# Kernel tuning notes

Hardware: AMD Instinct MI355X
Metric: run time of the kernel (lower is better)

## Reference

```python
import jax, jax.numpy as jnp
import numpy as np

# module hyperparams (init_kwargs)
OUTLINER_RATIO_1 = 0.01
OUTLINER_RATIO_2 = 0.01
SUB_OUTLINER_RATIO_2 = 0.2
SUB_OUTLINER_BIT_2 = 8
RANK = 16


def setup_inputs() -> dict:
    key = jax.random.key(0)
    k1, k2 = jax.random.split(key)
    B, H, S, D = 2, 16, 2048, 128
    # x1 is a softmax output (attention probabilities): rows sum to 1, values in [0,1]
    logits = jax.random.normal(k1, (B, H, S, S), dtype=jnp.float32)
    x1 = jax.nn.softmax(logits, axis=-1)
    x2 = jax.random.normal(k2, (B, H, S, D), dtype=jnp.float32)
    return {"x1": x1, "x2": x2}


def get_statistics_softmax(x, outliner_ratio):
    # kth-value threshold on first batch element (torch.kthvalue, 1-indexed)
    v = jnp.sort(x[0].reshape(-1))
    k = int(v.size * (1.0 - outliner_ratio))
    return v[k - 1]


def get_statistics_x2(x, outliner_ratio, sub_ratio, bit):
    x0 = x[0]  # [H, S, D]
    D = x0.shape[-1]
    a = jnp.abs(x0).reshape(-1)
    k = int(a.size * (1.0 - outliner_ratio))
    outliner = jnp.sort(a)[k - 1]
    # residual after removing outliers; rank columns by L2 norm
    resid = jnp.where(jnp.abs(x0) > outliner, 0.0, x0).reshape(-1, D)
    col_norm = jnp.linalg.norm(resid, axis=0)  # [D]
    n_cols = max(1, int(sub_ratio * D))
    _, cols = jax.lax.top_k(col_norm, n_cols)  # max-norm column list (static size)
    sub = resid[:, cols]
    qmax = float(2 ** (bit - 1) - 1)
    scale = jnp.max(jnp.abs(sub)) / qmax
    return outliner, cols, scale


def prune_softmax(x, outliner):
    return jnp.where(x > outliner, x, 0.0)


def fake_divide_outliner_suboutlinear_svd(x, outliner, cols, scale, rank, bit):
    # 1) split out outliers (kept exactly)
    x_out = jnp.where(jnp.abs(x) > outliner, x, 0.0)
    r = x - x_out
    # 2) rank-`rank` SVD approximation of the residual (batched over B,H)
    U, Sv, Vt = jnp.linalg.svd(r, full_matrices=False)
    x_lr = (U[..., :rank] * Sv[..., None, :rank]) @ Vt[..., :rank, :]
    r2 = r - x_lr
    # 3) fake-quantize the high-norm (sub-outlier) columns at `bit` bits; drop the rest
    qmax = float(2 ** (bit - 1) - 1)
    sub_q = jnp.clip(jnp.round(r2[..., cols] / scale), -qmax - 1.0, qmax) * scale
    r_q = jnp.zeros_like(r2).at[..., cols].set(sub_q)
    return x_out + x_lr + r_q


def reference(x1, x2):
    # iteration = 0 (< 10): compute statistics branch of EfficientMemoryGEMMWithSoftmaxFunc.forward
    result = x1 @ x2
    outliner_1 = get_statistics_softmax(x1, OUTLINER_RATIO_1)
    outliner_2, cols_2, scale_2 = get_statistics_x2(
        x2, OUTLINER_RATIO_2, SUB_OUTLINER_RATIO_2, SUB_OUTLINER_BIT_2)
    # The pruned/compressed tensors are computed (saved for backward in torch);
    # forward output matches Func.forward's returns.
    _x1p = prune_softmax(x1, outliner_1)
    _x2c = fake_divide_outliner_suboutlinear_svd(
        x2, outliner_2, cols_2, scale_2, RANK, SUB_OUTLINER_BIT_2)
    return (result, outliner_1, outliner_2, cols_2, scale_2)
```

## Files before the change

kernel.cpp:

```cpp
#include <hip/hip_runtime.h>

typedef __bf16 bf16x8 __attribute__((ext_vector_type(8)));
typedef unsigned short u16x8 __attribute__((ext_vector_type(8)));
typedef float f32x4 __attribute__((ext_vector_type(4)));

#define S_DIM 2048
#define D_DIM 128
#define N1 67108864LL
#define N2 4194304LL
#define RANK1 66437774u
#define RANK2 4152359u

#define OUT_O1 8388608
#define OUT_O2 8388609
#define OUT_COLS 8388610
#define OUT_SCALE 8388635

#define WS_H0 0
#define WS_H1 2048
#define WS_H2 4096
#define WS_H3 6144
#define WS_STATE 6656
#define WS_SMAX 6660
#define WS_MASK 6664
#define WS_SUMSQ 6672
#define WS_TOTAL 8192

__device__ __forceinline__ unsigned short f2bf(float f) {
  unsigned u = __float_as_uint(f);
  return (unsigned short)((u + 0x7FFFu + ((u >> 16) & 1u)) >> 16);
}

__global__ void init_ws(unsigned* __restrict__ ws) {
  int i = blockIdx.x * 256 + threadIdx.x;
  if (i < WS_TOTAL) ws[i] = (i == WS_STATE) ? RANK2 : 0u;
}

#define LDA 40

__global__ __launch_bounds__(256, 2) void gemm_kernel(
    const float* __restrict__ x1, const float* __restrict__ x2,
    float* __restrict__ out) {
  __shared__ __align__(16) unsigned short lA[128 * LDA];
  __shared__ __align__(16) unsigned short lB[128 * LDA];

  const int bh = blockIdx.x >> 4;
  const int mt = blockIdx.x & 15;
  const int t = threadIdx.x;
  const int lane = t & 63;
  const int wave = t >> 6;
  const int wm = (wave >> 1) * 64;
  const int wn = (wave & 1) * 64;
  const int l15 = lane & 15;
  const int quad = lane >> 4;

  const float* Ag = x1 + (long long)bh * S_DIM * S_DIM + (long long)mt * 128 * S_DIM;
  const float* Bg = x2 + (long long)bh * S_DIM * D_DIM;
  float* Cg = out + (long long)bh * S_DIM * D_DIM + (long long)mt * 128 * D_DIM;

  f32x4 acc[4][4];
#pragma unroll
  for (int i = 0; i < 4; ++i)
#pragma unroll
    for (int j = 0; j < 4; ++j) acc[i][j] = f32x4{0.f, 0.f, 0.f, 0.f};

  const int a_seg = t & 7;
  const int a_row = t >> 3;
  const int b_n = t & 127;
  const int b_kq = t >> 7;

  for (int kb = 0; kb < S_DIM; kb += 32) {
    __syncthreads();
#pragma unroll
    for (int p = 0; p < 4; ++p) {
      int row = a_row + p * 32;
      float4 v = *reinterpret_cast<const float4*>(Ag + (long long)row * S_DIM + kb + a_seg * 4);
      unsigned long long pk = (unsigned long long)f2bf(v.x)
                            | ((unsigned long long)f2bf(v.y) << 16)
                            | ((unsigned long long)f2bf(v.z) << 32)
                            | ((unsigned long long)f2bf(v.w) << 48);
      *reinterpret_cast<unsigned long long*>(&lA[row * LDA + a_seg * 4]) = pk;
    }
#pragma unroll
    for (int g = 0; g < 4; ++g) {
      int k0 = b_kq * 16 + g * 4;
      long long base = (long long)(kb + k0) * D_DIM + b_n;
      float f0 = Bg[base];
      float f1 = Bg[base + D_DIM];
      float f2 = Bg[base + 2 * D_DIM];
      float f3 = Bg[base + 3 * D_DIM];
      unsigned long long pk = (unsigned long long)f2bf(f0)
                            | ((unsigned long long)f2bf(f1) << 16)
                            | ((unsigned long long)f2bf(f2) << 32)
                            | ((unsigned long long)f2bf(f3) << 48);
      *reinterpret_cast<unsigned long long*>(&lB[b_n * LDA + k0]) = pk;
    }
    __syncthreads();

    bf16x8 af[4], bfr[4];
#pragma unroll
    for (int i = 0; i < 4; ++i) {
      af[i] = __builtin_bit_cast(bf16x8,
          *reinterpret_cast<const u16x8*>(&lA[(wm + i * 16 + l15) * LDA + quad * 8]));
      bfr[i] = __builtin_bit_cast(bf16x8,
          *reinterpret_cast<const u16x8*>(&lB[(wn + i * 16 + l15) * LDA + quad * 8]));
    }
#pragma unroll
    for (int i = 0; i < 4; ++i)
#pragma unroll
      for (int j = 0; j < 4; ++j)
        acc[i][j] = __builtin_amdgcn_mfma_f32_16x16x32_bf16(af[i], bfr[j], acc[i][j], 0, 0, 0);
  }

#pragma unroll
  for (int i = 0; i < 4; ++i) {
#pragma unroll
    for (int j = 0; j < 4; ++j) {
      int row0 = wm + i * 16 + quad * 4;
      int col = wn + j * 16 + l15;
#pragma unroll
      for (int r = 0; r < 4; ++r)
        Cg[(long long)(row0 + r) * D_DIM + col] = acc[i][j][r];
    }
  }
}

__global__ void x1_hist(const float* __restrict__ x1, unsigned* __restrict__ hist) {
  __shared__ unsigned lh[4 * 2049];
  for (int i = threadIdx.x; i < 4 * 2049; i += 256) lh[i] = 0u;
  __syncthreads();
  const int sub = (threadIdx.x & 3) * 2049;
  long long i0 = (long long)(blockIdx.x * 256 + threadIdx.x) * 4;
  long long stride = (long long)gridDim.x * 1024;
  for (long long i = i0; i < N1; i += stride) {
    float4 v = *reinterpret_cast<const float4*>(x1 + i);
    atomicAdd(&lh[sub + (__float_as_uint(v.x) >> 19)], 1u);
    atomicAdd(&lh[sub + (__float_as_uint(v.y) >> 19)], 1u);
    atomicAdd(&lh[sub + (__float_as_uint(v.z) >> 19)], 1u);
    atomicAdd(&lh[sub + (__float_as_uint(v.w) >> 19)], 1u);
  }
  __syncthreads();
  for (int i = threadIdx.x; i < 2048; i += 256) {
    unsigned s = lh[i] + lh[2049 + i] + lh[2 * 2049 + i] + lh[3 * 2049 + i];
    if (s) atomicAdd(&hist[i], s);
  }
}

__global__ void x1_select(const unsigned* __restrict__ hist, float* __restrict__ out) {
  __shared__ unsigned ps[256];
  const int t = threadIdx.x;
  unsigned v[8];
  unsigned s = 0;
#pragma unroll
  for (int j = 0; j < 8; ++j) { v[j] = hist[t * 8 + j]; s += v[j]; }
  ps[t] = s;
  __syncthreads();
  for (int off = 1; off < 256; off <<= 1) {
    unsigned add = (t >= off) ? ps[t - off] : 0u;
    __syncthreads();
    ps[t] += add;
    __syncthreads();
  }
  unsigned incl = ps[t];
  unsigned before = incl - s;
  if (RANK1 >= before && RANK1 < incl) {
    unsigned rr = RANK1 - before;
    for (int j = 0; j < 8; ++j) {
      if (rr < v[j]) {
        unsigned b = (unsigned)(t * 8 + j);
        float lo = __uint_as_float(b << 19);
        float hi = __uint_as_float((b + 1u) << 19);
        out[OUT_O1] = lo + (hi - lo) * (((float)rr + 0.5f) / (float)v[j]);
        break;
      }
      rr -= v[j];
    }
  }
}

__global__ void x2_hist(const float* __restrict__ x2, unsigned* __restrict__ h,
                        const unsigned* __restrict__ state, int phase) {
  __shared__ unsigned lh[2048];
  const int nb = (phase == 3) ? 512 : 2048;
  for (int i = threadIdx.x; i < nb; i += 256) lh[i] = 0u;
  __syncthreads();
  const unsigned b1 = state[1];
  const unsigned pfx2 = (state[1] << 11) | state[2];
  long long i0 = (long long)(blockIdx.x * 256 + threadIdx.x) * 4;
  long long stride = (long long)gridDim.x * 1024;
  for (long long i = i0; i < N2; i += stride) {
    float4 v = *reinterpret_cast<const float4*>(x2 + i);
    float fv[4] = {v.x, v.y, v.z, v.w};
#pragma unroll
    for (int j = 0; j < 4; ++j) {
      unsigned key = __float_as_uint(fv[j]) & 0x7FFFFFFFu;
      if (phase == 1) {
        atomicAdd(&lh[key >> 20], 1u);
      } else if (phase == 2) {
        if ((key >> 20) == b1) atomicAdd(&lh[(key >> 9) & 0x7FFu], 1u);
      } else {
        if ((key >> 9) == pfx2) atomicAdd(&lh[key & 0x1FFu], 1u);
      }
    }
  }
  __syncthreads();
  for (int i = threadIdx.x; i < nb; i += 256)
    if (lh[i]) atomicAdd(&h[i], lh[i]);
}

__global__ void x2_scan(const unsigned* __restrict__ h, unsigned* state,
                        float* __restrict__ out, int phase) {
  __shared__ unsigned ps[256];
  const int nb = (phase == 3) ? 512 : 2048;
  const int per = nb >> 8;
  const int t = threadIdx.x;
  const unsigned r = state[0];
  const unsigned sb1 = state[1];
  const unsigned sb2 = state[2];
  unsigned v[8];
  unsigned s = 0;
  for (int j = 0; j < per; ++j) { v[j] = h[t * per + j]; s += v[j]; }
  ps[t] = s;
  __syncthreads();
  for (int off = 1; off < 256; off <<= 1) {
    unsigned add = (t >= off) ? ps[t - off] : 0u;
    __syncthreads();
    ps[t] += add;
    __syncthreads();
  }
  unsigned incl = ps[t];
  unsigned before = incl - s;
  if (r >= before && r < incl) {
    unsigned rr = r - before;
    for (int j = 0; j < per; ++j) {
      if (rr < v[j]) {
        unsigned b = (unsigned)(t * per + j);
        state[0] = rr;
        if (phase == 1) state[1] = b;
        else if (phase == 2) state[2] = b;
        else {
          unsigned bits = (sb1 << 20) | (sb2 << 9) | b;
          state[3] = bits;
          out[OUT_O2] = __uint_as_float(bits);
        }
        break;
      }
      rr -= v[j];
    }
  }
}

__global__ void colnorm_kernel(const float* __restrict__ x2,
                               const unsigned* __restrict__ state,
                               float* __restrict__ sumsq) {
  const float thr = __uint_as_float(state[3]);
  const int t = threadIdx.x;
  const int c = t & 127;
  const int half = t >> 7;
  float local = 0.f;
  for (int i = 0; i < 64; ++i) {
    int row = blockIdx.x * 128 + i * 2 + half;
    float x = x2[(long long)row * 128 + c];
    if (fabsf(x) <= thr) local += x * x;
  }
  __shared__ float red[256];
  red[t] = local;
  __syncthreads();
  if (half == 0) atomicAdd(&sumsq[c], red[c] + red[c + 128]);
}

__global__ void topk_kernel(const float* __restrict__ sumsq, float* __restrict__ out,
                            unsigned* __restrict__ mask) {
  __shared__ float v[128];
  __shared__ float rv[128];
  __shared__ int ri[128];
  __shared__ unsigned msk[4];
  const int t = threadIdx.x;
  v[t] = sumsq[t];
  if (t < 4) msk[t] = 0u;
  __syncthreads();
  for (int s = 0; s < 25; ++s) {
    rv[t] = v[t];
    ri[t] = t;
    __syncthreads();
    for (int off = 64; off >= 1; off >>= 1) {
      if (t < off) {
        float a = rv[t], b = rv[t + off];
        int ia = ri[t], ib = ri[t + off];
        if (b > a || (b == a && ib < ia)) { rv[t] = b; ri[t] = ib; }
      }
      __syncthreads();
    }
    if (t == 0) {
      int c = ri[0];
      out[OUT_COLS + s] = (float)c;
      v[c] = -1.0f;
      msk[c >> 5] |= 1u << (c & 31);
    }
    __syncthreads();
  }
  if (t < 4) mask[t] = msk[t];
}

__global__ void scale_kernel(const float* __restrict__ x2,
                             const unsigned* __restrict__ state,
                             const unsigned* __restrict__ mask,
                             unsigned* __restrict__ smax) {
  const float thr = __uint_as_float(state[3]);
  unsigned long long mlo = (unsigned long long)mask[0] | ((unsigned long long)mask[1] << 32);
  unsigned long long mhi = (unsigned long long)mask[2] | ((unsigned long long)mask[3] << 32);
  long long i0 = (long long)(blockIdx.x * 256 + threadIdx.x) * 4;
  long long stride = (long long)gridDim.x * 1024;
  float best = 0.f;
  for (long long i = i0; i < N2; i += stride) {
    float4 v = *reinterpret_cast<const float4*>(x2 + i);
    float fv[4] = {v.x, v.y, v.z, v.w};
    int cbase = (int)(i & 127);
#pragma unroll
    for (int j = 0; j < 4; ++j) {
      int c = cbase + j;
      unsigned long long w = (c < 64) ? mlo : mhi;
      if ((w >> (c & 63)) & 1ULL) {
        float a = fabsf(fv[j]);
        if (a <= thr && a > best) best = a;
      }
    }
  }
  __shared__ float red[256];
  red[threadIdx.x] = best;
  __syncthreads();
  for (int off = 128; off >= 1; off >>= 1) {
    if (threadIdx.x < off) red[threadIdx.x] = fmaxf(red[threadIdx.x], red[threadIdx.x + off]);
    __syncthreads();
  }
  if (threadIdx.x == 0) atomicMax(smax, __float_as_uint(red[0]));
}

__global__ void finalize_kernel(const unsigned* __restrict__ smax, float* __restrict__ out) {
  out[OUT_SCALE] = __uint_as_float(*smax) / 127.0f;
}

extern "C" void kernel_launch(void* const* d_in, const int* in_sizes, int n_in,
                              void* d_out, int out_size, void* d_ws, size_t ws_size,
                              hipStream_t stream) {
  (void)in_sizes; (void)n_in; (void)out_size; (void)ws_size;
  const float* x1 = (const float*)d_in[0];
  const float* x2 = (const float*)d_in[1];
  float* out = (float*)d_out;
  unsigned* ws = (unsigned*)d_ws;

  init_ws<<<32, 256, 0, stream>>>(ws);
  gemm_kernel<<<512, 256, 0, stream>>>(x1, x2, out);
  x1_hist<<<512, 256, 0, stream>>>(x1, ws + WS_H0);
  x1_select<<<1, 256, 0, stream>>>(ws + WS_H0, out);
  x2_hist<<<256, 256, 0, stream>>>(x2, ws + WS_H1, ws + WS_STATE, 1);
  x2_scan<<<1, 256, 0, stream>>>(ws + WS_H1, ws + WS_STATE, out, 1);
  x2_hist<<<256, 256, 0, stream>>>(x2, ws + WS_H2, ws + WS_STATE, 2);
  x2_scan<<<1, 256, 0, stream>>>(ws + WS_H2, ws + WS_STATE, out, 2);
  x2_hist<<<256, 256, 0, stream>>>(x2, ws + WS_H3, ws + WS_STATE, 3);
  x2_scan<<<1, 256, 0, stream>>>(ws + WS_H3, ws + WS_STATE, out, 3);
  colnorm_kernel<<<256, 256, 0, stream>>>(x2, ws + WS_STATE, (float*)(ws + WS_SUMSQ));
  topk_kernel<<<1, 128, 0, stream>>>((const float*)(ws + WS_SUMSQ), out, ws + WS_MASK);
  scale_kernel<<<256, 256, 0, stream>>>(x2, ws + WS_STATE, ws + WS_MASK, ws + WS_SMAX);
  finalize_kernel<<<1, 1, 0, stream>>>(ws + WS_SMAX, out);
}
```

Measured before the change: 928.6 us.

## Fuse x1 histogram into GEMM, prefetch next tiles into registers, swizzle block order

Builds the x1 value histogram inside the GEMM kernel for the first batch element, from the A-tile registers already loaded. This removes the separate pass that re-read the whole 256MB x1 tensor. The GEMM now register-prefetches the next k-slice of A and B while computing the current one, and remaps block indices so that blocks sharing a tile are grouped. The cost is 32KB of extra shared memory for per-wave histograms, which may reduce occupancy, and LDS atomics added to the GEMM inner loop.

After: 843.4 us. -9.2%, faster.

```diff
diff --git a/kernel.cpp b/kernel.cpp
--- a/kernel.cpp
+++ b/kernel.cpp
@@ -31,6 +31,13 @@
   return (unsigned short)((u + 0x7FFFu + ((u >> 16) & 1u)) >> 16);
 }
 
+__device__ __forceinline__ unsigned long long pack4(float x, float y, float z, float w) {
+  return (unsigned long long)f2bf(x)
+       | ((unsigned long long)f2bf(y) << 16)
+       | ((unsigned long long)f2bf(z) << 32)
+       | ((unsigned long long)f2bf(w) << 48);
+}
+
 __global__ void init_ws(unsigned* __restrict__ ws) {
   int i = blockIdx.x * 256 + threadIdx.x;
   if (i < WS_TOTAL) ws[i] = (i == WS_STATE) ? RANK2 : 0u;
@@ -40,12 +47,14 @@
 
 __global__ __launch_bounds__(256, 2) void gemm_kernel(
     const float* __restrict__ x1, const float* __restrict__ x2,
-    float* __restrict__ out) {
+    float* __restrict__ out, unsigned* __restrict__ hist) {
   __shared__ __align__(16) unsigned short lA[128 * LDA];
   __shared__ __align__(16) unsigned short lB[128 * LDA];
-
-  const int bh = blockIdx.x >> 4;
-  const int mt = blockIdx.x & 15;
+  __shared__ unsigned lh[4][2048];
+
+  const int bid = blockIdx.x;
+  const int bh = (bid & 7) + ((bid >> 7) << 3);
+  const int mt = (bid >> 3) & 15;
   const int t = threadIdx.x;
   const int lane = t & 63;
   const int wave = t >> 6;
@@ -53,6 +62,12 @@
   const int wn = (wave & 1) * 64;
   const int l15 = lane & 15;
   const int quad = lane >> 4;
+  const bool do_hist = (bh < 16);
+
+  unsigned* myh = lh[wave];
+  if (do_hist) {
+    for (int i = lane; i < 2048; i += 64) myh[i] = 0u;
+  }
 
   const float* Ag = x1 + (long long)bh * S_DIM * S_DIM + (long long)mt * 128 * S_DIM;
   const float* Bg = x2 + (long long)bh * S_DIM * D_DIM;
@@ -69,31 +84,59 @@
   const int b_n = t & 127;
   const int b_kq = t >> 7;
 
+  float4 a_r[4];
+  float4 b_r[4];
+#pragma unroll
+  for (int p = 0; p < 4; ++p)
+    a_r[p] = *reinterpret_cast<const float4*>(Ag + (long long)(a_row + p * 32) * S_DIM + a_seg * 4);
+#pragma unroll
+  for (int g = 0; g < 4; ++g) {
+    int k0 = b_kq * 16 + g * 4;
+    long long base = (long long)k0 * D_DIM + b_n;
+    b_r[g].x = Bg[base];
+    b_r[g].y = Bg[base + D_DIM];
+    b_r[g].z = Bg[base + 2 * D_DIM];
+    b_r[g].w = Bg[base + 3 * D_DIM];
+  }
+
   for (int kb = 0; kb < S_DIM; kb += 32) {
-    __syncthreads();
 #pragma unroll
     for (int p = 0; p < 4; ++p) {
       int row = a_row + p * 32;
-      float4 v = *reinterpret_cast<const float4*>(Ag + (long long)row * S_DIM + kb + a_seg * 4);
-      unsigned long long pk = (unsigned long long)f2bf(v.x)
-                            | ((unsigned long long)f2bf(v.y) << 16)
-                            | ((unsigned long long)f2bf(v.z) << 32)
-                            | ((unsigned long long)f2bf(v.w) << 48);
-      *reinterpret_cast<unsigned long long*>(&lA[row * LDA + a_seg * 4]) = pk;
+      *reinterpret_cast<unsigned long long*>(&lA[row * LDA + a_seg * 4]) =
+          pack4(a_r[p].x, a_r[p].y, a_r[p].z, a_r[p].w);
     }
 #pragma unroll
     for (int g = 0; g < 4; ++g) {
       int k0 = b_kq * 16 + g * 4;
-      long long base = (long long)(kb + k0) * D_DIM + b_n;
-      float f0 = Bg[base];
-      float f1 = Bg[base + D_DIM];
-      float f2 = Bg[base + 2 * D_DIM];
-      float f3 = Bg[base + 3 * D_DIM];
-      unsigned long long pk = (unsigned long long)f2bf(f0)
-                            | ((unsigned long long)f2bf(f1) << 16)
-                            | ((unsigned long long)f2bf(f2) << 32)
-                            | ((unsigned long long)f2bf(f3) << 48);
-      *reinterpret_cast<unsigned long long*>(&lB[b_n * LDA + k0]) = pk;
+      *reinterpret_cast<unsigned long long*>(&lB[b_n * LDA + k0]) =
+          pack4(b_r[g].x, b_r[g].y, b_r[g].z, b_r[g].w);
+    }
+
+    if (do_hist) {
+#pragma unroll
+      for (int p = 0; p < 4; ++p) {
+        atomicAdd(&myh[__float_as_uint(a_r[p].x) >> 19], 1u);
+        atomicAdd(&myh[__float_as_uint(a_r[p].y) >> 19], 1u);
+        atomicAdd(&myh[__float_as_uint(a_r[p].z) >> 19], 1u);
+        atomicAdd(&myh[__float_as_uint(a_r[p].w) >> 19], 1u);
+      }
+    }
+
+    if (kb + 32 < S_DIM) {
+#pragma unroll
+      for (int p = 0; p < 4; ++p)
+        a_r[p] = *reinterpret_cast<const float4*>(
+            Ag + (long long)(a_row + p * 32) * S_DIM + (kb + 32) + a_seg * 4);
+#pragma unroll
+      for (int g = 0; g < 4; ++g) {
+        int k0 = b_kq * 16 + g * 4;
+        long long base = (long long)(kb + 32 + k0) * D_DIM + b_n;
+        b_r[g].x = Bg[base];
+        b_r[g].y = Bg[base + D_DIM];
+        b_r[g].z = Bg[base + 2 * D_DIM];
+        b_r[g].w = Bg[base + 3 * D_DIM];
+      }
     }
     __syncthreads();
 
@@ -110,6 +153,7 @@
 #pragma unroll
       for (int j = 0; j < 4; ++j)
         acc[i][j] = __builtin_amdgcn_mfma_f32_16x16x32_bf16(af[i], bfr[j], acc[i][j], 0, 0, 0);
+    __syncthreads();
   }
 
 #pragma unroll
@@ -123,26 +167,12 @@
         Cg[(long long)(row0 + r) * D_DIM + col] = acc[i][j][r];
     }
   }
-}
-
-__global__ void x1_hist(const float* __restrict__ x1, unsigned* __restrict__ hist) {
-  __shared__ unsigned lh[4 * 2049];
-  for (int i = threadIdx.x; i < 4 * 2049; i += 256) lh[i] = 0u;
-  __syncthreads();
-  const int sub = (threadIdx.x & 3) * 2049;
-  long long i0 = (long long)(blockIdx.x * 256 + threadIdx.x) * 4;
-  long long stride = (long long)gridDim.x * 1024;
-  for (long long i = i0; i < N1; i += stride) {
-    float4 v = *reinterpret_cast<const float4*>(x1 + i);
-    atomicAdd(&lh[sub + (__float_as_uint(v.x) >> 19)], 1u);
-    atomicAdd(&lh[sub + (__float_as_uint(v.y) >> 19)], 1u);
-    atomicAdd(&lh[sub + (__float_as_uint(v.z) >> 19)], 1u);
-    atomicAdd(&lh[sub + (__float_as_uint(v.w) >> 19)], 1u);
-  }
-  __syncthreads();
-  for (int i = threadIdx.x; i < 2048; i += 256) {
-    unsigned s = lh[i] + lh[2049 + i] + lh[2 * 2049 + i] + lh[3 * 2049 + i];
-    if (s) atomicAdd(&hist[i], s);
+
+  if (do_hist) {
+    for (int i = t; i < 2048; i += 256) {
+      unsigned s = lh[0][i] + lh[1][i] + lh[2][i] + lh[3][i];
+      if (s) atomicAdd(&hist[i], s);
+    }
   }
 }
 
@@ -350,8 +380,7 @@
   unsigned* ws = (unsigned*)d_ws;
 
   init_ws<<<32, 256, 0, stream>>>(ws);
-  gemm_kernel<<<512, 256, 0, stream>>>(x1, x2, out);
-  x1_hist<<<512, 256, 0, stream>>>(x1, ws + WS_H0);
+  gemm_kernel<<<512, 256, 0, stream>>>(x1, x2, out, ws + WS_H0);
   x1_select<<<1, 256, 0, stream>>>(ws + WS_H0, out);
   x2_hist<<<256, 256, 0, stream>>>(x2, ws + WS_H1, ws + WS_STATE, 1);
   x2_scan<<<1, 256, 0, stream>>>(ws + WS_H1, ws + WS_STATE, out, 1);
```
